# Optimization experiments

Measured on AMD Instinct MI355X. Metric: run time of the kernel, lower is better.

## Reference

```python
import jax, jax.numpy as jnp
import numpy as np

N_PROMPT = 20
N_SAMPLES = 10000


def setup_inputs() -> dict:
    key = jax.random.key(0)
    k1, k2, k3, k4 = jax.random.split(key, 4)
    B, L, D = 32, 512, 768
    sample_id_tensor = jax.random.randint(k1, (B,), 0, N_SAMPLES, dtype=jnp.int64)
    input_embeds = jax.random.normal(k2, (B, L, D), dtype=jnp.float32)
    attention_mask = jax.random.randint(k3, (B, L), 0, 2, dtype=jnp.int32)
    # learned parameter: per-sample prompt embeddings, std=0.02 init
    prompt_embeddings = 0.02 * jax.random.normal(k4, (N_SAMPLES, N_PROMPT, D), dtype=jnp.float32)
    return {
        "sample_id_tensor": sample_id_tensor,
        "input_embeds": input_embeds,
        "attention_mask": attention_mask,
        "prompt_embeddings": prompt_embeddings,
    }


def reference(sample_id_tensor, input_embeds, attention_mask, prompt_embeddings):
    # sample_id_to_index is identity (sample_id_list = range(N_SAMPLES))
    prompts = prompt_embeddings[sample_id_tensor]            # [B, n_prompt, D]
    pad = attention_mask == 0                                # [B, L]
    # rank of each pad slot among pad slots of its row (0-based)
    rank = jnp.cumsum(pad.astype(jnp.int32), axis=1) - 1     # [B, L]
    take = pad & (rank < N_PROMPT)                           # first min(K, n_prompt) pads
    safe_rank = jnp.clip(rank, 0, N_PROMPT - 1)
    # gather prompt row `rank` for each position (only used where `take`)
    gathered = jnp.take_along_axis(prompts, safe_rank[:, :, None], axis=1)  # [B, L, D]
    inputs_embeds_new = jnp.where(take[:, :, None], gathered, input_embeds)
    attention_mask_new = jnp.where(take, jnp.ones_like(attention_mask), attention_mask)
    return (inputs_embeds_new, attention_mask_new)
```

## Files before the change

kernel.cpp:

```cpp
#include <hip/hip_runtime.h>

#define B_DIM 32
#define L_DIM 512
#define D_DIM 768
#define N_PROMPT 20
#define D4 (D_DIM / 4)
#define TOTAL4 (B_DIM * L_DIM * D4)
#define COPY_BLOCK 256
#define COPY_GRID 2048
#define COPY_ITERS (TOTAL4 / (COPY_BLOCK * COPY_GRID))

__global__ __launch_bounds__(COPY_BLOCK) void copy_kernel(
        const float4* __restrict__ in, float4* __restrict__ out) {
    size_t idx = (size_t)blockIdx.x * COPY_BLOCK + threadIdx.x;
    const size_t stride = (size_t)COPY_GRID * COPY_BLOCK;
#pragma unroll
    for (int i = 0; i < COPY_ITERS; ++i) {
        out[idx + i * stride] = in[idx + i * stride];
    }
}

__global__ __launch_bounds__(256) void scan_scatter_kernel(
        const int* __restrict__ mask,
        const int* __restrict__ sids,
        const float4* __restrict__ prompts,
        float4* __restrict__ out_embeds,
        float* __restrict__ out_mask) {
    const int b    = blockIdx.x;
    const int tid  = threadIdx.x;
    const int lane = tid & 63;
    const int wave = tid >> 6;

    __shared__ int s_pos[N_PROMPT];
    __shared__ int s_cnt;

    const int row_off = b * L_DIM;

    if (wave == 0) {
        int base = 0;
        for (int chunk = 0; chunk < L_DIM; chunk += 64) {
            const int l = chunk + lane;
            const int m = mask[row_off + l];
            const bool pad = (m == 0);
            const unsigned long long bal = __ballot(pad);
            const unsigned long long lower =
                bal & ((1ULL << lane) - 1ULL);
            const int rank = base + __popcll(lower);
            const bool take = pad && (rank < N_PROMPT);
            out_mask[row_off + l] = take ? 1.0f : (float)m;
            if (take) s_pos[rank] = l;
            base += __popcll(bal);
        }
        if (lane == 0) s_cnt = (base < N_PROMPT) ? base : N_PROMPT;
    }
    __syncthreads();

    const int cnt = s_cnt;
    if (cnt == 0) return;
    const int sid = sids[b];
    const size_t pbase = (size_t)sid * N_PROMPT * D4;

    const int total = cnt * D4;
    for (int i = tid; i < total; i += 256) {
        const int k = i / D4;
        const int d = i - k * D4;
        out_embeds[((size_t)(row_off + s_pos[k])) * D4 + d] =
            prompts[pbase + (size_t)k * D4 + d];
    }
}

extern "C" void kernel_launch(void* const* d_in, const int* in_sizes, int n_in,
                              void* d_out, int out_size, void* d_ws, size_t ws_size,
                              hipStream_t stream) {
    const int*   sids    = (const int*)d_in[0];
    const float* embeds  = (const float*)d_in[1];
    const int*   mask    = (const int*)d_in[2];
    const float* prompts = (const float*)d_in[3];

    float* out_embeds = (float*)d_out;
    float* out_mask   = out_embeds + (size_t)B_DIM * L_DIM * D_DIM;

    copy_kernel<<<COPY_GRID, COPY_BLOCK, 0, stream>>>(
        (const float4*)embeds, (float4*)out_embeds);

    scan_scatter_kernel<<<B_DIM, 256, 0, stream>>>(
        mask, sids, (const float4*)prompts, (float4*)out_embeds, out_mask);
}
```

Measured before the change: 702.8 us.

## Fuse copy and prompt scatter into one kernel with per-block redundant mask scan

Replaces the separate full-tensor copy kernel and per-row scan/scatter kernel with one kernel. Each block covers 8 rows of one batch entry, every wave recomputes the pad-rank scan for that batch row, and each output row is read either from the prompt table or from the input embeddings. This drops the second launch and the double write to the 20 prompt rows, and removes the serial dependency between the two kernels. The cost is 2048 blocks each redundantly scanning a 512-entry mask row.

```diff
diff --git a/kernel.cpp b/kernel.cpp
--- a/kernel.cpp
+++ b/kernel.cpp
@@ -5,67 +5,59 @@
 #define D_DIM 768
 #define N_PROMPT 20
 #define D4 (D_DIM / 4)
-#define TOTAL4 (B_DIM * L_DIM * D4)
-#define COPY_BLOCK 256
-#define COPY_GRID 2048
-#define COPY_ITERS (TOTAL4 / (COPY_BLOCK * COPY_GRID))
+#define SEGS 64
+#define ROWS_PB (L_DIM / SEGS)
+#define BLOCK 256
 
-__global__ __launch_bounds__(COPY_BLOCK) void copy_kernel(
-        const float4* __restrict__ in, float4* __restrict__ out) {
-    size_t idx = (size_t)blockIdx.x * COPY_BLOCK + threadIdx.x;
-    const size_t stride = (size_t)COPY_GRID * COPY_BLOCK;
-#pragma unroll
-    for (int i = 0; i < COPY_ITERS; ++i) {
-        out[idx + i * stride] = in[idx + i * stride];
-    }
-}
-
-__global__ __launch_bounds__(256) void scan_scatter_kernel(
+__global__ __launch_bounds__(BLOCK) void fused_kernel(
         const int* __restrict__ mask,
         const int* __restrict__ sids,
+        const float4* __restrict__ embeds,
         const float4* __restrict__ prompts,
         float4* __restrict__ out_embeds,
         float* __restrict__ out_mask) {
-    const int b    = blockIdx.x;
+    const int blk  = blockIdx.x;
+    const int b    = blk >> 6;
+    const int seg  = blk & 63;
     const int tid  = threadIdx.x;
     const int lane = tid & 63;
     const int wave = tid >> 6;
 
-    __shared__ int s_pos[N_PROMPT];
-    __shared__ int s_cnt;
+    const int row_off    = b * L_DIM;
+    const int chunk_mine = seg >> 3;
+    const int sub        = (seg & 7) * 8;
 
-    const int row_off = b * L_DIM;
+    int base   = 0;
+    int s_mine = -1;
+    for (int chunk = 0; chunk < 8; ++chunk) {
+        const int l   = (chunk << 6) + lane;
+        const int m   = mask[row_off + l];
+        const bool pad = (m == 0);
+        const unsigned long long bal = __ballot(pad);
+        const int rank = base + __popcll(bal & ((1ULL << lane) - 1ULL));
+        const bool take = pad && (rank < N_PROMPT);
+        if (chunk == chunk_mine) {
+            s_mine = take ? rank : -1;
+            if (wave == 0 && lane >= sub && lane < sub + ROWS_PB)
+                out_mask[row_off + l] = take ? 1.0f : (float)m;
+        }
+        base += __popcll(bal);
+    }
 
-    if (wave == 0) {
-        int base = 0;
-        for (int chunk = 0; chunk < L_DIM; chunk += 64) {
-            const int l = chunk + lane;
-            const int m = mask[row_off + l];
-            const bool pad = (m == 0);
-            const unsigned long long bal = __ballot(pad);
-            const unsigned long long lower =
-                bal & ((1ULL << lane) - 1ULL);
-            const int rank = base + __popcll(lower);
-            const bool take = pad && (rank < N_PROMPT);
-            out_mask[row_off + l] = take ? 1.0f : (float)m;
-            if (take) s_pos[rank] = l;
-            base += __popcll(bal);
-        }
-        if (lane == 0) s_cnt = (base < N_PROMPT) ? base : N_PROMPT;
-    }
-    __syncthreads();
+    const int sid = sids[b];
+    const size_t pbase = (size_t)sid * (N_PROMPT * D4);
+    const size_t obase = ((size_t)(row_off + seg * ROWS_PB)) * D4;
 
-    const int cnt = s_cnt;
-    if (cnt == 0) return;
-    const int sid = sids[b];
-    const size_t pbase = (size_t)sid * N_PROMPT * D4;
-
-    const int total = cnt * D4;
-    for (int i = tid; i < total; i += 256) {
-        const int k = i / D4;
-        const int d = i - k * D4;
-        out_embeds[((size_t)(row_off + s_pos[k])) * D4 + d] =
-            prompts[pbase + (size_t)k * D4 + d];
+#pragma unroll
+    for (int it = 0; it < 6; ++it) {
+        const int row = wave * 2 + it / 3;
+        const int off = (it % 3) * 64 + lane;
+        const int s   = __shfl(s_mine, sub + row);
+        const size_t oidx = obase + (size_t)row * D4 + off;
+        float4 v;
+        if (s >= 0) v = prompts[pbase + (size_t)s * D4 + off];
+        else        v = embeds[oidx];
+        out_embeds[oidx] = v;
     }
 }
 
@@ -80,9 +72,7 @@
     float* out_embeds = (float*)d_out;
     float* out_mask   = out_embeds + (size_t)B_DIM * L_DIM * D_DIM;
 
-    copy_kernel<<<COPY_GRID, COPY_BLOCK, 0, stream>>>(
-        (const float4*)embeds, (float4*)out_embeds);
-
-    scan_scatter_kernel<<<B_DIM, 256, 0, stream>>>(
-        mask, sids, (const float4*)prompts, (float4*)out_embeds, out_mask);
+    fused_kernel<<<B_DIM * SEGS, BLOCK, 0, stream>>>(
+        mask, sids, (const float4*)embeds, (const float4*)prompts,
+        (float4*)out_embeds, out_mask);
 }
```

Result: no change. 689.3 us (-1.9%).
